# Performance work log

Hardware: AMD Instinct MI355X
Metric: run time of the kernel (lower is better)

Reference implementation:

```python
import jax, jax.numpy as jnp
import numpy as np

IN_F, OUT_F, NUM_GRIDS, BATCH = 2048, 2048, 8, 4096


def setup_inputs() -> dict:
    key = jax.random.key(0)
    ks = jax.random.split(key, 5)
    x = jax.random.normal(ks[0], (BATCH, IN_F), dtype=jnp.float32)
    # kaiming_uniform_(a=sqrt(5)) on Linear weight -> U(-b, b), b = 1/sqrt(in_features)
    bound = 1.0 / np.sqrt(IN_F)
    base_w = jax.random.uniform(ks[1], (OUT_F, IN_F), dtype=jnp.float32, minval=-bound, maxval=bound)
    base_b = jnp.zeros((OUT_F,), dtype=jnp.float32)
    spline_weight = 0.1 * jax.random.normal(ks[2], (OUT_F, IN_F, NUM_GRIDS), dtype=jnp.float32)
    grid = jnp.linspace(-2.0, 2.0, NUM_GRIDS, dtype=jnp.float32)
    adaptive_gate = jnp.ones((OUT_F,), dtype=jnp.float32)
    feature_importance = jnp.ones((IN_F,), dtype=jnp.float32)
    return {"x": x, "base_w": base_w, "base_b": base_b,
            "spline_weight": spline_weight, "grid": grid,
            "adaptive_gate": adaptive_gate, "feature_importance": feature_importance}


def reference(x, base_w, base_b, spline_weight, grid, adaptive_gate, feature_importance):
    # feature gating
    x_weighted = x * jax.nn.sigmoid(feature_importance)[None, :]          # [b, i]
    # base path: Linear
    base_output = x_weighted @ base_w.T + base_b                          # [b, o]
    # spline path: RBF basis over grid
    x_norm = jnp.tanh(x_weighted)                                         # [b, i]
    basis = jnp.exp(-((x_norm[:, :, None] - grid[None, None, :]) ** 2) * 2.0)  # [b, i, g]
    # F.normalize(p=1, dim=-1): divide by L1 norm clamped to eps
    denom = jnp.maximum(jnp.sum(jnp.abs(basis), axis=-1, keepdims=True), 1e-12)
    basis = basis / denom
    spline_output = jnp.einsum('big,oig->bo', basis, spline_weight)       # [b, o]
    gate = jax.nn.sigmoid(adaptive_gate)[None, :]                         # [1, o]
    return gate * spline_output + (1.0 - gate) * base_output
```

## Files before the change

kernel.cpp:

```cpp
#include <hip/hip_runtime.h>
#include <hip/hip_bf16.h>

#define IN_F   2048
#define OUT_F  2048
#define NG     8
#define BATCH  4096
#define KDIM   (IN_F * (NG + 1))
#define BK     64
#define NT     (KDIM / BK)
#define BM     256
#define BN     128
#define ASZ    (BM * BK * 2)
#define BSZ    (BN * BK * 2)
#define BUFSZ  (ASZ + BSZ)

typedef short bf16x8 __attribute__((ext_vector_type(8)));
typedef float f32x4  __attribute__((ext_vector_type(4)));
typedef __attribute__((address_space(3))) unsigned char       lds_u8;
typedef const __attribute__((address_space(1))) unsigned char glb_u8;

__device__ __forceinline__ float sigmoidf_(float v) {
    return 1.0f / (1.0f + __expf(-v));
}

__device__ __forceinline__ unsigned short f2bf(float f) {
    unsigned int u = __builtin_bit_cast(unsigned int, f);
    u = (u + 0x7fffu + ((u >> 16) & 1u)) >> 16;
    return (unsigned short)u;
}

__global__ __launch_bounds__(256) void act_kernel(
    const float* __restrict__ x, const float* __restrict__ fi,
    const float* __restrict__ gr, unsigned short* __restrict__ Abf)
{
    const int base = blockIdx.x * 1024;
    const int tid  = threadIdx.x;
    const int b    = base >> 11;
    const float4 g0 = *(const float4*)gr;
    const float4 g1 = *(const float4*)(gr + 4);
    unsigned short* rowp = Abf + (size_t)b * KDIM;

#pragma unroll
    for (int e = 0; e < 4; ++e) {
        const int idx = base + tid + e * 256;
        const int i   = idx & (IN_F - 1);
        const float s  = sigmoidf_(fi[i]);
        const float xw = x[idx] * s;
        const float ex = __expf(2.0f * xw);
        const float xn = (ex - 1.0f) / (ex + 1.0f);

        float ev[NG];
        float d;
        d = xn - g0.x; ev[0] = __expf(-2.0f * d * d);
        d = xn - g0.y; ev[1] = __expf(-2.0f * d * d);
        d = xn - g0.z; ev[2] = __expf(-2.0f * d * d);
        d = xn - g0.w; ev[3] = __expf(-2.0f * d * d);
        d = xn - g1.x; ev[4] = __expf(-2.0f * d * d);
        d = xn - g1.y; ev[5] = __expf(-2.0f * d * d);
        d = xn - g1.z; ev[6] = __expf(-2.0f * d * d);
        d = xn - g1.w; ev[7] = __expf(-2.0f * d * d);
        float denom = ((ev[0] + ev[1]) + (ev[2] + ev[3])) +
                      ((ev[4] + ev[5]) + (ev[6] + ev[7]));
        const float rinv = 1.0f / fmaxf(denom, 1e-12f);

        union { unsigned short us[8]; int4 v; } pk;
#pragma unroll
        for (int g = 0; g < NG; ++g) pk.us[g] = f2bf(ev[g] * rinv);
        *(int4*)(rowp + i * NG) = pk.v;
        rowp[IN_F * NG + i] = f2bf(xw);
    }
}

__global__ __launch_bounds__(256) void wprep_kernel(
    const float* __restrict__ bw, const float* __restrict__ sw,
    const float* __restrict__ ag, unsigned short* __restrict__ Wbf)
{
    const int base = blockIdx.x * 1024;
    const int tid  = threadIdx.x;
    const int o    = base >> 11;
    const float gate = sigmoidf_(ag[o]);
    const float og   = 1.0f - gate;
    unsigned short* rowp = Wbf + (size_t)o * KDIM;

#pragma unroll
    for (int e = 0; e < 4; ++e) {
        const int idx = base + tid + e * 256;
        const int i   = idx & (IN_F - 1);
        const float4 s0 = *(const float4*)(sw + (size_t)idx * NG);
        const float4 s1 = *(const float4*)(sw + (size_t)idx * NG + 4);
        union { unsigned short us[8]; int4 v; } pk;
        pk.us[0] = f2bf(gate * s0.x); pk.us[1] = f2bf(gate * s0.y);
        pk.us[2] = f2bf(gate * s0.z); pk.us[3] = f2bf(gate * s0.w);
        pk.us[4] = f2bf(gate * s1.x); pk.us[5] = f2bf(gate * s1.y);
        pk.us[6] = f2bf(gate * s1.z); pk.us[7] = f2bf(gate * s1.w);
        *(int4*)(rowp + i * NG) = pk.v;
        rowp[IN_F * NG + i] = f2bf(og * bw[idx]);
    }
}

#define MFMA(d, a, b) d = __builtin_amdgcn_mfma_f32_16x16x32_bf16(a, b, d, 0, 0, 0)

#define PHASE_MID()                                            \
    __builtin_amdgcn_sched_barrier(0);                         \
    __builtin_amdgcn_s_barrier();                              \
    asm volatile("s_waitcnt lgkmcnt(0)" ::: "memory");         \
    __builtin_amdgcn_sched_barrier(0);

#define PHASE_END()                                            \
    __builtin_amdgcn_sched_barrier(0);                         \
    __builtin_amdgcn_s_barrier();

#define LDA(kk, m) (*(const bf16x8*)(lds + curBase + (oA##m ^ ((kk) << 6))))
#define LDB(kk, n) (*(const bf16x8*)(lds + curBase + (oB##n ^ ((kk) << 6))))

#define GLA(j) __builtin_amdgcn_global_load_lds((glb_u8*)(aS##j + ko), \
                   (lds_u8*)(lds + stBase + aO##j), 16, 0, 0)
#define GLB(j) __builtin_amdgcn_global_load_lds((glb_u8*)(bS##j + ko), \
                   (lds_u8*)(lds + stBase + bO##j), 16, 0, 0)

__global__ __launch_bounds__(512, 2) void gemm_kernel(
    const unsigned short* __restrict__ A, const unsigned short* __restrict__ B,
    const float* __restrict__ bb, const float* __restrict__ ag,
    float* __restrict__ C)
{
    __shared__ __align__(16) unsigned char lds[3 * BUFSZ];

    const int tid = threadIdx.x;
    const int bid = blockIdx.x;
    const int swz = ((bid & 7) << 5) + (bid >> 3);
    const int bm = swz >> 4, bn = swz & 15;

    const int lane = tid & 63, wid = tid >> 6;
    const int wm = wid >> 1, wn = wid & 1;
    const int fr = lane & 15, kg = lane >> 4;

#define MKSA(j)                                                         \
    const int eA##j = tid + (j) * 512;                                  \
    const int rA_##j = eA##j >> 3, cA_##j = (eA##j & 7) ^ (rA_##j & 7); \
    const unsigned short* aS##j = A + (size_t)(bm * BM + rA_##j) * KDIM + cA_##j * 8; \
    const int aO##j = eA##j * 16;
    MKSA(0) MKSA(1) MKSA(2) MKSA(3)
#define MKSB(j)                                                         \
    const int eB##j = tid + (j) * 512;                                  \
    const int rB_##j = eB##j >> 3, cB_##j = (eB##j & 7) ^ (rB_##j & 7); \
    const unsigned short* bS##j = B + (size_t)(bn * BN + rB_##j) * KDIM + cB_##j * 8; \
    const int bO##j = ASZ + eB##j * 16;
    MKSB(0) MKSB(1)

#define MKOA(m)                                                \
    const int rAm##m = wm * 64 + (m) * 16 + fr;                \
    const int oA##m = rAm##m * 128 + ((kg ^ (rAm##m & 7)) << 4);
    MKOA(0) MKOA(1) MKOA(2) MKOA(3)
#define MKOB(n)                                                \
    const int rBn##n = wn * 64 + (n) * 16 + fr;                \
    const int oB##n = ASZ + rBn##n * 128 + ((kg ^ (rBn##n & 7)) << 4);
    MKOB(0) MKOB(1) MKOB(2) MKOB(3)

    f32x4 acc[4][4] = {};

    {
        const int stBase = 0; const long ko = 0;
        GLA(0); GLA(1); GLA(2); GLA(3); GLB(0); GLB(1);
    }
    {
        const int stBase = BUFSZ; const long ko = BK;
        GLA(0); GLA(1); GLA(2); GLA(3); GLB(0); GLB(1);
    }
    asm volatile("s_waitcnt vmcnt(6)" ::: "memory");
    __builtin_amdgcn_sched_barrier(0);
    __builtin_amdgcn_s_barrier();

    int curBase = 0;
    for (int t = 0; t < NT; ++t) {
        const int stBase = (curBase >= BUFSZ) ? (curBase - BUFSZ)
                                              : (curBase + 2 * BUFSZ);
        const bool doSt = (t + 2) < NT;
        const long ko = (long)(t + 2) * BK;

        {
            bf16x8 va0 = LDA(0, 0), va1 = LDA(0, 1), va2 = LDA(0, 2), va3 = LDA(0, 3);
            bf16x8 vb0 = LDB(0, 0), vb1 = LDB(0, 1), vb2 = LDB(0, 2), vb3 = LDB(0, 3);
            if (doSt) { GLA(0); GLA(1); GLA(2); }
            PHASE_MID();
            __builtin_amdgcn_s_setprio(1);
            MFMA(acc[0][0], va0, vb0); MFMA(acc[0][1], va0, vb1);
            MFMA(acc[0][2], va0, vb2); MFMA(acc[0][3], va0, vb3);
            MFMA(acc[1][0], va1, vb0); MFMA(acc[1][1], va1, vb1);
            MFMA(acc[1][2], va1, vb2); MFMA(acc[1][3], va1, vb3);
            MFMA(acc[2][0], va2, vb0); MFMA(acc[2][1], va2, vb1);
            MFMA(acc[2][2], va2, vb2); MFMA(acc[2][3], va2, vb3);
            MFMA(acc[3][0], va3, vb0); MFMA(acc[3][1], va3, vb1);
            MFMA(acc[3][2], va3, vb2); MFMA(acc[3][3], va3, vb3);
            __builtin_amdgcn_s_setprio(0);
            PHASE_END();
        }

        {
            bf16x8 va0 = LDA(1, 0), va1 = LDA(1, 1), va2 = LDA(1, 2), va3 = LDA(1, 3);
            bf16x8 vb0 = LDB(1, 0), vb1 = LDB(1, 1), vb2 = LDB(1, 2), vb3 = LDB(1, 3);
            if (doSt) { GLA(3); GLB(0); GLB(1); }
            PHASE_MID();
            __builtin_amdgcn_s_setprio(1);
            MFMA(acc[0][0], va0, vb0); MFMA(acc[0][1], va0, vb1);
            MFMA(acc[0][2], va0, vb2); MFMA(acc[0][3], va0, vb3);
            MFMA(acc[1][0], va1, vb0); MFMA(acc[1][1], va1, vb1);
            MFMA(acc[1][2], va1, vb2); MFMA(acc[1][3], va1, vb3);
            MFMA(acc[2][0], va2, vb0); MFMA(acc[2][1], va2, vb1);
            MFMA(acc[2][2], va2, vb2); MFMA(acc[2][3], va2, vb3);
            MFMA(acc[3][0], va3, vb0); MFMA(acc[3][1], va3, vb1);
            MFMA(acc[3][2], va3, vb2); MFMA(acc[3][3], va3, vb3);
            __builtin_amdgcn_s_setprio(0);
            if (doSt) { asm volatile("s_waitcnt vmcnt(6)" ::: "memory"); }
            else      { asm volatile("s_waitcnt vmcnt(0)" ::: "memory"); }
            PHASE_END();
        }

        curBase = (curBase == 2 * BUFSZ) ? 0 : (curBase + BUFSZ);
    }

    const int colb = bn * BN + wn * 64;
    const int rowb = bm * BM + wm * 64;
#pragma unroll
    for (int n = 0; n < 4; ++n) {
        const int col = colb + n * 16 + fr;
        const float gate = sigmoidf_(ag[col]);
        const float bias = (1.0f - gate) * bb[col];
#pragma unroll
        for (int m = 0; m < 4; ++m) {
            const int r0 = rowb + m * 16 + kg * 4;
#pragma unroll
            for (int j = 0; j < 4; ++j)
                C[(size_t)(r0 + j) * OUT_F + col] = acc[m][n][j] + bias;
        }
    }
}

extern "C" void kernel_launch(void* const* d_in, const int* in_sizes, int n_in,
                              void* d_out, int out_size, void* d_ws, size_t ws_size,
                              hipStream_t stream)
{
    const float* x  = (const float*)d_in[0];
    const float* bw = (const float*)d_in[1];
    const float* bb = (const float*)d_in[2];
    const float* sw = (const float*)d_in[3];
    const float* gr = (const float*)d_in[4];
    const float* ag = (const float*)d_in[5];
    const float* fi = (const float*)d_in[6];
    float* out = (float*)d_out;

    unsigned short* Abf = (unsigned short*)d_ws;
    unsigned short* Wbf = Abf + (size_t)BATCH * KDIM;

    const size_t need = ((size_t)BATCH + OUT_F) * KDIM * sizeof(unsigned short);
    if (ws_size < need) return;

    act_kernel<<<BATCH * IN_F / 1024, 256, 0, stream>>>(x, fi, gr, Abf);
    wprep_kernel<<<OUT_F * IN_F / 1024, 256, 0, stream>>>(bw, sw, ag, Wbf);
    gemm_kernel<<<(BATCH / BM) * (OUT_F / BN), 512, 0, stream>>>(Abf, Wbf, bb, ag, out);
}
```

Before: 547.3 us.

## Split K across warp pairs with 128x64 warp tiles and LDS reduction

Reorganises the 8 warps so pairs split the 64-wide K slice (each warp takes half) while each warp covers a 128x64 output tile instead of 64x64. All global-to-LDS stores are issued in a single phase per iteration, and the two partial accumulators are summed through LDS in the epilogue. This raises MFMA work per LDS fragment load and halves the barriers per K tile. In exchange it doubles accumulator registers (128 floats per lane), which threatens occupancy at 2 blocks per CU, and it adds an LDS reduction at the end.

```diff
diff --git a/kernel.cpp b/kernel.cpp
--- a/kernel.cpp
+++ b/kernel.cpp
@@ -110,8 +110,8 @@
     __builtin_amdgcn_sched_barrier(0);                         \
     __builtin_amdgcn_s_barrier();
 
-#define LDA(kk, m) (*(const bf16x8*)(lds + curBase + (oA##m ^ ((kk) << 6))))
-#define LDB(kk, n) (*(const bf16x8*)(lds + curBase + (oB##n ^ ((kk) << 6))))
+#define LDA(m) (*(const bf16x8*)(lds + curBase + oA##m))
+#define LDB(n) (*(const bf16x8*)(lds + curBase + oB##n))
 
 #define GLA(j) __builtin_amdgcn_global_load_lds((glb_u8*)(aS##j + ko), \
                    (lds_u8*)(lds + stBase + aO##j), 16, 0, 0)
@@ -131,8 +131,9 @@
     const int bm = swz >> 4, bn = swz & 15;
 
     const int lane = tid & 63, wid = tid >> 6;
-    const int wm = wid >> 1, wn = wid & 1;
+    const int ks = wid & 1, wn = (wid >> 1) & 1, wm = wid >> 2;
     const int fr = lane & 15, kg = lane >> 4;
+    const int kq = 4 * ks + kg;
 
 #define MKSA(j)                                                         \
     const int eA##j = tid + (j) * 512;                                  \
@@ -148,15 +149,15 @@
     MKSB(0) MKSB(1)
 
 #define MKOA(m)                                                \
-    const int rAm##m = wm * 64 + (m) * 16 + fr;                \
-    const int oA##m = rAm##m * 128 + ((kg ^ (rAm##m & 7)) << 4);
-    MKOA(0) MKOA(1) MKOA(2) MKOA(3)
+    const int rAm##m = wm * 128 + (m) * 16 + fr;               \
+    const int oA##m = rAm##m * 128 + ((kq ^ (rAm##m & 7)) << 4);
+    MKOA(0) MKOA(1) MKOA(2) MKOA(3) MKOA(4) MKOA(5) MKOA(6) MKOA(7)
 #define MKOB(n)                                                \
     const int rBn##n = wn * 64 + (n) * 16 + fr;                \
-    const int oB##n = ASZ + rBn##n * 128 + ((kg ^ (rBn##n & 7)) << 4);
+    const int oB##n = ASZ + rBn##n * 128 + ((kq ^ (rBn##n & 7)) << 4);
     MKOB(0) MKOB(1) MKOB(2) MKOB(3)
 
-    f32x4 acc[4][4] = {};
+    f32x4 acc[8][4] = {};
 
     {
         const int stBase = 0; const long ko = 0;
@@ -177,60 +178,63 @@
         const bool doSt = (t + 2) < NT;
         const long ko = (long)(t + 2) * BK;
 
-        {
-            bf16x8 va0 = LDA(0, 0), va1 = LDA(0, 1), va2 = LDA(0, 2), va3 = LDA(0, 3);
-            bf16x8 vb0 = LDB(0, 0), vb1 = LDB(0, 1), vb2 = LDB(0, 2), vb3 = LDB(0, 3);
-            if (doSt) { GLA(0); GLA(1); GLA(2); }
-            PHASE_MID();
-            __builtin_amdgcn_s_setprio(1);
-            MFMA(acc[0][0], va0, vb0); MFMA(acc[0][1], va0, vb1);
-            MFMA(acc[0][2], va0, vb2); MFMA(acc[0][3], va0, vb3);
-            MFMA(acc[1][0], va1, vb0); MFMA(acc[1][1], va1, vb1);
-            MFMA(acc[1][2], va1, vb2); MFMA(acc[1][3], va1, vb3);
-            MFMA(acc[2][0], va2, vb0); MFMA(acc[2][1], va2, vb1);
-            MFMA(acc[2][2], va2, vb2); MFMA(acc[2][3], va2, vb3);
-            MFMA(acc[3][0], va3, vb0); MFMA(acc[3][1], va3, vb1);
-            MFMA(acc[3][2], va3, vb2); MFMA(acc[3][3], va3, vb3);
-            __builtin_amdgcn_s_setprio(0);
-            PHASE_END();
-        }
-
-        {
-            bf16x8 va0 = LDA(1, 0), va1 = LDA(1, 1), va2 = LDA(1, 2), va3 = LDA(1, 3);
-            bf16x8 vb0 = LDB(1, 0), vb1 = LDB(1, 1), vb2 = LDB(1, 2), vb3 = LDB(1, 3);
-            if (doSt) { GLA(3); GLB(0); GLB(1); }
-            PHASE_MID();
-            __builtin_amdgcn_s_setprio(1);
-            MFMA(acc[0][0], va0, vb0); MFMA(acc[0][1], va0, vb1);
-            MFMA(acc[0][2], va0, vb2); MFMA(acc[0][3], va0, vb3);
-            MFMA(acc[1][0], va1, vb0); MFMA(acc[1][1], va1, vb1);
-            MFMA(acc[1][2], va1, vb2); MFMA(acc[1][3], va1, vb3);
-            MFMA(acc[2][0], va2, vb0); MFMA(acc[2][1], va2, vb1);
-            MFMA(acc[2][2], va2, vb2); MFMA(acc[2][3], va2, vb3);
-            MFMA(acc[3][0], va3, vb0); MFMA(acc[3][1], va3, vb1);
-            MFMA(acc[3][2], va3, vb2); MFMA(acc[3][3], va3, vb3);
-            __builtin_amdgcn_s_setprio(0);
-            if (doSt) { asm volatile("s_waitcnt vmcnt(6)" ::: "memory"); }
-            else      { asm volatile("s_waitcnt vmcnt(0)" ::: "memory"); }
-            PHASE_END();
-        }
+        bf16x8 va0 = LDA(0), va1 = LDA(1), va2 = LDA(2), va3 = LDA(3);
+        bf16x8 va4 = LDA(4), va5 = LDA(5), va6 = LDA(6), va7 = LDA(7);
+        bf16x8 vb0 = LDB(0), vb1 = LDB(1), vb2 = LDB(2), vb3 = LDB(3);
+        if (doSt) { GLA(0); GLA(1); GLA(2); GLA(3); GLB(0); GLB(1); }
+        PHASE_MID();
+        __builtin_amdgcn_s_setprio(1);
+        MFMA(acc[0][0], va0, vb0); MFMA(acc[0][1], va0, vb1);
+        MFMA(acc[0][2], va0, vb2); MFMA(acc[0][3], va0, vb3);
+        MFMA(acc[1][0], va1, vb0); MFMA(acc[1][1], va1, vb1);
+        MFMA(acc[1][2], va1, vb2); MFMA(acc[1][3], va1, vb3);
+        MFMA(acc[2][0], va2, vb0); MFMA(acc[2][1], va2, vb1);
+        MFMA(acc[2][2], va2, vb2); MFMA(acc[2][3], va2, vb3);
+        MFMA(acc[3][0], va3, vb0); MFMA(acc[3][1], va3, vb1);
+        MFMA(acc[3][2], va3, vb2); MFMA(acc[3][3], va3, vb3);
+        MFMA(acc[4][0], va4, vb0); MFMA(acc[4][1], va4, vb1);
+        MFMA(acc[4][2], va4, vb2); MFMA(acc[4][3], va4, vb3);
+        MFMA(acc[5][0], va5, vb0); MFMA(acc[5][1], va5, vb1);
+        MFMA(acc[5][2], va5, vb2); MFMA(acc[5][3], va5, vb3);
+        MFMA(acc[6][0], va6, vb0); MFMA(acc[6][1], va6, vb1);
+        MFMA(acc[6][2], va6, vb2); MFMA(acc[6][3], va6, vb3);
+        MFMA(acc[7][0], va7, vb0); MFMA(acc[7][1], va7, vb1);
+        MFMA(acc[7][2], va7, vb2); MFMA(acc[7][3], va7, vb3);
+        __builtin_amdgcn_s_setprio(0);
+        if (doSt) { asm volatile("s_waitcnt vmcnt(6)" ::: "memory"); }
+        else      { asm volatile("s_waitcnt vmcnt(0)" ::: "memory"); }
+        PHASE_END();
 
         curBase = (curBase == 2 * BUFSZ) ? 0 : (curBase + BUFSZ);
     }
 
-    const int colb = bn * BN + wn * 64;
-    const int rowb = bm * BM + wm * 64;
-#pragma unroll
-    for (int n = 0; n < 4; ++n) {
-        const int col = colb + n * 16 + fr;
-        const float gate = sigmoidf_(ag[col]);
-        const float bias = (1.0f - gate) * bb[col];
-#pragma unroll
-        for (int m = 0; m < 4; ++m) {
-            const int r0 = rowb + m * 16 + kg * 4;
-#pragma unroll
-            for (int j = 0; j < 4; ++j)
-                C[(size_t)(r0 + j) * OUT_F + col] = acc[m][n][j] + bias;
+    const int slot = wm * 2 + wn;
+    if (ks == 1) {
+#pragma unroll
+        for (int m = 0; m < 8; ++m)
+#pragma unroll
+            for (int n = 0; n < 4; ++n)
+                *(f32x4*)(lds + slot * 32768 + (m * 4 + n) * 1024 + lane * 16)
+                    = acc[m][n];
+    }
+    __syncthreads();
+    if (ks == 0) {
+        const int colb = bn * BN + wn * 64;
+        const int rowb = bm * BM + wm * 128;
+#pragma unroll
+        for (int n = 0; n < 4; ++n) {
+            const int col = colb + n * 16 + fr;
+            const float gate = sigmoidf_(ag[col]);
+            const float bias = (1.0f - gate) * bb[col];
+#pragma unroll
+            for (int m = 0; m < 8; ++m) {
+                const f32x4 part =
+                    *(const f32x4*)(lds + slot * 32768 + (m * 4 + n) * 1024 + lane * 16);
+                const int r0 = rowb + m * 16 + kg * 4;
+#pragma unroll
+                for (int j = 0; j < 4; ++j)
+                    C[(size_t)(r0 + j) * OUT_F + col] = acc[m][n][j] + part[j] + bias;
+            }
         }
     }
 }
```

Result: slower. 562.9 us (+2.9%).
